# Optimization experiments

Measured on AMD Instinct MI355X. Metric: run time of the kernel, lower is better.

The kernel has to match this reference:

```python
import jax, jax.numpy as jnp
import numpy as np

M, K, N = 4096, 4096, 12288
GS = 128                 # quantization group size
G = K // GS              # number of groups
PACK = 8                 # int4 values per int32


def _pack_nibbles(key, shape_packed, axis_len):
    # generate random int4 values and pack 8 per int32 (bit-faithful GPTQ layout)
    nib = jax.random.randint(key, shape_packed[:1] + (PACK,) + shape_packed[1:], 0, 16, dtype=jnp.uint32)
    shifts = (jnp.arange(PACK, dtype=jnp.uint32) * 4)[None, :, None]
    return jnp.sum(nib << shifts, axis=1).astype(jnp.int32)


def setup_inputs() -> dict:
    key = jax.random.key(0)
    k1, k2, k3, k4, k5 = jax.random.split(key, 5)
    x = jax.random.normal(k1, (M, K), dtype=jnp.float32) * 0.05
    qweight = _pack_nibbles(k2, (K // PACK, N), K)          # [K/8, N] int32
    qzeros = _pack_nibbles(k3, (G, N // PACK), N)           # [G, N/8] int32
    scales = jax.random.uniform(k4, (G, N), dtype=jnp.float32, minval=0.001, maxval=0.01)
    bias = jax.random.normal(k5, (N,), dtype=jnp.float32) * 0.01
    return {"x": x, "qweight": qweight, "qzeros": qzeros, "scales": scales, "bias": bias}


def _unpack_rows(q):
    # [R, C] int32 -> [R*8, C] int4 values unpacked along rows
    shifts = (jnp.arange(PACK, dtype=jnp.uint32) * 4)[None, :, None]
    nib = (q.astype(jnp.uint32)[:, None, :] >> shifts) & jnp.uint32(0xF)
    return nib.reshape(q.shape[0] * PACK, q.shape[1])


def _unpack_cols(q):
    # [R, C] int32 -> [R, C*8] int4 values unpacked along columns
    shifts = (jnp.arange(PACK, dtype=jnp.uint32) * 4)[None, None, :]
    nib = (q.astype(jnp.uint32)[:, :, None] >> shifts) & jnp.uint32(0xF)
    return nib.reshape(q.shape[0], q.shape[1] * PACK)


def reference(x, qweight, qzeros, scales, bias):
    # dequantize: w[k,n] = (q[k,n] - (z[g,n]+1)) * s[g,n],  g = k // GS
    q = _unpack_rows(qweight).astype(jnp.float32)                    # [K, N]
    z = (_unpack_cols(qzeros).astype(jnp.float32) + 1.0)             # [G, N]
    s = scales                                                       # [G, N]
    w = (q.reshape(G, GS, N) - z[:, None, :]) * s[:, None, :]        # [G, GS, N]
    w = w.reshape(K, N)
    return x @ w + bias
```

## Files before the change

kernel.cpp:

```cpp
#include <hip/hip_runtime.h>
#include <hip/hip_bf16.h>

namespace {
constexpr int Md = 4096, Kd = 4096, Nd = 12288;
constexpr int BM = 256, BN = 128, BK = 64;
constexpr int TK = Kd / BK;
constexpr int THREADS = 512;
constexpr size_t A_BYTES = (size_t)Md * Kd * 2;
constexpr int AS_T = BM * BK;
constexpr int BS_T = BN * BK;
constexpr int LDS_BYTES = (2 * AS_T + BS_T) * 2;

typedef __attribute__((ext_vector_type(4))) float f4;
typedef __attribute__((ext_vector_type(8))) _Float16 h8;
typedef __attribute__((ext_vector_type(2))) _Float16 h2;

constexpr unsigned M4  = 0x000F000Fu;
constexpr unsigned MAG = 0x64006400u;

__device__ __forceinline__ unsigned pkrtz(float lo, float hi) {
  return __builtin_bit_cast(unsigned, __builtin_amdgcn_cvt_pkrtz(lo, hi));
}

__global__ __launch_bounds__(256)
void cvtA_kernel(const float* __restrict__ X, unsigned short* __restrict__ Xb, int n8) {
  int i = blockIdx.x * blockDim.x + threadIdx.x;
  const int stride = gridDim.x * blockDim.x;
  for (; i < n8; i += stride) {
    const f4* p = (const f4*)X + (size_t)i * 2;
    f4 a = p[0], b = p[1];
    uint4 o;
    o.x = pkrtz(a[0], b[0]);
    o.y = pkrtz(a[1], b[1]);
    o.z = pkrtz(a[2], b[2]);
    o.w = pkrtz(a[3], b[3]);
    ((uint4*)Xb)[i] = o;
  }
}

template<bool AWS>
__global__ __launch_bounds__(THREADS, 4)
void qgemm5(const float* __restrict__ X, const unsigned short* __restrict__ Xb,
            const int* __restrict__ QW, const int* __restrict__ QZ,
            const float* __restrict__ SC, const float* __restrict__ BS,
            float* __restrict__ OUT)
{
  extern __shared__ char smem[];
  unsigned short* As = (unsigned short*)smem;
  unsigned short* Bs = (unsigned short*)(smem + 2 * AS_T * 2);

  const int nwg = gridDim.x, cpx = nwg >> 3, b = blockIdx.x;
  const int swz = (b & 7) * cpx + (b >> 3);
  const int bm = swz / (Nd / BN), bn = swz % (Nd / BN);
  const int m0 = bm * BM, n0 = bn * BN;

  const int tid = threadIdx.x, lane = tid & 63, wid = tid >> 6;
  const int wr = wid >> 1, wc = wid & 1;
  const int n_l = tid & 127;
  const int k8b = (tid >> 7) * 2;
  const int nab = n0 + n_l;

  f4 acc[4][4];
  #pragma unroll
  for (int i = 0; i < 4; ++i)
    #pragma unroll
    for (int j = 0; j < 4; ++j) acc[i][j] = {0.0f, 0.0f, 0.0f, 0.0f};

  auto stageA = [&](int t, int buf) {
    #pragma unroll
    for (int i = 0; i < 4; ++i) {
      const int c = i * THREADS + tid;
      const int r = c >> 3, kbl = c & 7;
      const unsigned short* src = Xb + (size_t)(m0 + r) * Kd + t * BK + ((kbl ^ (r & 7)) << 3);
      __builtin_amdgcn_global_load_lds(
          (const __attribute__((address_space(1))) unsigned*)src,
          (__attribute__((address_space(3))) unsigned*)(As + buf * AS_T + c * 8),
          16, 0, 0);
    }
  };
  auto stageA_f = [&](int t, int buf) {
    #pragma unroll
    for (int i = 0; i < 4; ++i) {
      const int c = i * THREADS + tid;
      const int r = c >> 3, kbl = c & 7;
      const f4* src = (const f4*)(X + (size_t)(m0 + r) * Kd + t * BK + ((kbl ^ (r & 7)) << 3));
      f4 a = src[0], bb = src[1];
      uint4 o;
      o.x = pkrtz(a[0], bb[0]); o.y = pkrtz(a[1], bb[1]);
      o.z = pkrtz(a[2], bb[2]); o.w = pkrtz(a[3], bb[3]);
      *(uint4*)(As + buf * AS_T + c * 8) = o;
    }
  };

  auto loadB = [&](int t, int* w, unsigned& hs2, unsigned& hz2) {
    const int* qp = QW + (size_t)(t * 8 + k8b) * Nd + nab;
    w[0] = qp[0];
    w[1] = qp[Nd];
    const int g = t >> 1;
    const float s = SC[(size_t)g * Nd + nab];
    const int z32 = QZ[(size_t)g * (Nd / 8) + (nab >> 3)];
    const int z = (z32 >> ((nab & 7) * 4)) & 15;
    const unsigned hz = 0x6400u + (unsigned)z + 1u;
    hz2 = hz * 0x10001u;
    const unsigned short hs = __builtin_bit_cast(unsigned short, (_Float16)s);
    hs2 = (unsigned)hs * 0x10001u;
  };
  auto writeB = [&](const int* w, unsigned hs2, unsigned hz2) {
    const h2 vz = __builtin_bit_cast(h2, hz2);
    const h2 vs = __builtin_bit_cast(h2, hs2);
    #pragma unroll
    for (int i = 0; i < 2; ++i) {
      const unsigned q = (unsigned)w[i];
      const int k8 = k8b + i;
      const unsigned p0 = (q & M4) | MAG;
      const unsigned p1 = ((q >> 4) & M4) | MAG;
      const unsigned p2 = ((q >> 8) & M4) | MAG;
      const unsigned p3 = ((q >> 12) & M4) | MAG;
      const h2 f0 = (__builtin_bit_cast(h2, p0) - vz) * vs;
      const h2 f1 = (__builtin_bit_cast(h2, p1) - vz) * vs;
      const h2 f2 = (__builtin_bit_cast(h2, p2) - vz) * vs;
      const h2 f3 = (__builtin_bit_cast(h2, p3) - vz) * vs;
      uint4 o;
      o.x = __builtin_bit_cast(unsigned, f0);
      o.y = __builtin_bit_cast(unsigned, f1);
      o.z = __builtin_bit_cast(unsigned, f2);
      o.w = __builtin_bit_cast(unsigned, f3);
      *(uint4*)(Bs + n_l * BK + ((k8 ^ (n_l & 7)) << 3)) = o;
    }
  };

  auto mfma_tile = [&](int cb) {
    const unsigned short* Ab = As + cb * AS_T;
    #pragma unroll
    for (int ks = 0; ks < 2; ++ks) {
      h8 af[4], bf[4];
      const int kb = ks * 4 + (lane >> 4);
      #pragma unroll
      for (int mi = 0; mi < 4; ++mi) {
        const int r = wr * 64 + mi * 16 + (lane & 15);
        af[mi] = *(const h8*)&Ab[r * BK + ((kb ^ (r & 7)) << 3)];
      }
      #pragma unroll
      for (int ni = 0; ni < 4; ++ni) {
        const int cc = wc * 64 + ni * 16 + (lane & 15);
        bf[ni] = *(const h8*)&Bs[cc * BK + ((kb ^ (cc & 7)) << 3)];
      }
      #pragma unroll
      for (int mi = 0; mi < 4; ++mi)
        #pragma unroll
        for (int ni = 0; ni < 4; ++ni)
          acc[mi][ni] = __builtin_amdgcn_mfma_f32_16x16x32_f16(af[mi], bf[ni], acc[mi][ni], 0, 0, 0);
    }
  };

  int bw[2]; unsigned sHS, sHZ;
  int nbw[2]; unsigned nHS, nHZ;

  if constexpr (AWS) stageA(0, 0); else stageA_f(0, 0);
  loadB(0, bw, sHS, sHZ);
  writeB(bw, sHS, sHZ);
  __syncthreads();

  for (int t = 0; t < TK; ++t) {
    const int cb = t & 1;
    if (t + 1 < TK) {
      if constexpr (AWS) stageA(t + 1, cb ^ 1);
      loadB(t + 1, nbw, nHS, nHZ);
    }
    mfma_tile(cb);
    __syncthreads();
    if (t + 1 < TK) {
      if constexpr (!AWS) stageA_f(t + 1, cb ^ 1);
      writeB(nbw, nHS, nHZ);
    }
    __syncthreads();
  }

  #pragma unroll
  for (int ni = 0; ni < 4; ++ni) {
    const int gn = n0 + wc * 64 + ni * 16 + (lane & 15);
    const float bv = BS[gn];
    #pragma unroll
    for (int mi = 0; mi < 4; ++mi) {
      const int gm = m0 + wr * 64 + mi * 16 + ((lane >> 4) << 2);
      #pragma unroll
      for (int j = 0; j < 4; ++j)
        OUT[(size_t)(gm + j) * Nd + gn] = acc[mi][ni][j] + bv;
    }
  }
}
}

extern "C" void kernel_launch(void* const* d_in, const int* in_sizes, int n_in,
                              void* d_out, int out_size, void* d_ws, size_t ws_size,
                              hipStream_t stream) {
  const float* x  = (const float*)d_in[0];
  const int*   qw = (const int*)d_in[1];
  const int*   qz = (const int*)d_in[2];
  const float* sc = (const float*)d_in[3];
  const float* bs = (const float*)d_in[4];
  float* out = (float*)d_out;

  (void)hipFuncSetAttribute((const void*)qgemm5<true>,
                            hipFuncAttributeMaxDynamicSharedMemorySize, LDS_BYTES);
  (void)hipFuncSetAttribute((const void*)qgemm5<false>,
                            hipFuncAttributeMaxDynamicSharedMemorySize, LDS_BYTES);

  dim3 grid((Md / BM) * (Nd / BN));
  if (ws_size >= A_BYTES) {
    unsigned short* xb = (unsigned short*)d_ws;
    const int n8 = Md * Kd / 8;
    cvtA_kernel<<<2048, 256, 0, stream>>>(x, xb, n8);
    qgemm5<true><<<grid, dim3(THREADS), LDS_BYTES, stream>>>(x, xb, qw, qz, sc, bs, out);
  } else {
    qgemm5<false><<<grid, dim3(THREADS), LDS_BYTES, stream>>>(x, nullptr, qw, qz, sc, bs, out);
  }
}
```

Baseline: 419.3 us.

## Pre-dequantize weights to fp16 in workspace and run plain fp16 GEMM

Adds a separate kernel that dequantizes the int4 weights into an N-major fp16 buffer in the workspace. The main GEMM then streams both A and B into LDS with async global-to-LDS loads instead of dequantizing in registers each K step. The GEMM also moves to 256 threads, with each wave covering 128 rows and holding 8x4 accumulators. The aim is to take dequant ALU work and register staging out of the inner loop. The cost is an extra 96MB write and read of fp16 weights, more registers, and a larger workspace; when the workspace is too small the old path is kept as a fallback.

New measurement: 485.4 us. 1.16x slower.

```diff
diff --git a/kernel.cpp b/kernel.cpp
--- a/kernel.cpp
+++ b/kernel.cpp
@@ -5,11 +5,12 @@
 constexpr int Md = 4096, Kd = 4096, Nd = 12288;
 constexpr int BM = 256, BN = 128, BK = 64;
 constexpr int TK = Kd / BK;
-constexpr int THREADS = 512;
 constexpr size_t A_BYTES = (size_t)Md * Kd * 2;
+constexpr size_t W_BYTES = (size_t)Kd * Nd * 2;
 constexpr int AS_T = BM * BK;
 constexpr int BS_T = BN * BK;
-constexpr int LDS_BYTES = (2 * AS_T + BS_T) * 2;
+constexpr int LDS_MAIN = (2 * AS_T + BS_T) * 2;
+constexpr int LDS_FB   = (2 * AS_T + BS_T) * 2;
 
 typedef __attribute__((ext_vector_type(4))) float f4;
 typedef __attribute__((ext_vector_type(8))) _Float16 h8;
@@ -23,23 +24,168 @@
 }
 
 __global__ __launch_bounds__(256)
-void cvtA_kernel(const float* __restrict__ X, unsigned short* __restrict__ Xb, int n8) {
+void cvtA_nat(const float* __restrict__ X, unsigned short* __restrict__ Xb, int n8) {
   int i = blockIdx.x * blockDim.x + threadIdx.x;
   const int stride = gridDim.x * blockDim.x;
   for (; i < n8; i += stride) {
     const f4* p = (const f4*)X + (size_t)i * 2;
     f4 a = p[0], b = p[1];
     uint4 o;
-    o.x = pkrtz(a[0], b[0]);
-    o.y = pkrtz(a[1], b[1]);
-    o.z = pkrtz(a[2], b[2]);
-    o.w = pkrtz(a[3], b[3]);
+    o.x = pkrtz(a[0], a[1]); o.y = pkrtz(a[2], a[3]);
+    o.z = pkrtz(b[0], b[1]); o.w = pkrtz(b[2], b[3]);
     ((uint4*)Xb)[i] = o;
   }
 }
 
+__global__ __launch_bounds__(256)
+void cvtA_perm(const float* __restrict__ X, unsigned short* __restrict__ Xb, int n8) {
+  int i = blockIdx.x * blockDim.x + threadIdx.x;
+  const int stride = gridDim.x * blockDim.x;
+  for (; i < n8; i += stride) {
+    const f4* p = (const f4*)X + (size_t)i * 2;
+    f4 a = p[0], b = p[1];
+    uint4 o;
+    o.x = pkrtz(a[0], b[0]); o.y = pkrtz(a[1], b[1]);
+    o.z = pkrtz(a[2], b[2]); o.w = pkrtz(a[3], b[3]);
+    ((uint4*)Xb)[i] = o;
+  }
+}
+
+__global__ __launch_bounds__(256)
+void dequantW(const int* __restrict__ QW, const int* __restrict__ QZ,
+              const float* __restrict__ SC, unsigned short* __restrict__ Wt)
+{
+  __shared__ unsigned short L[64][68];
+  const int kb = blockIdx.x & 63;
+  const int nb = blockIdx.x >> 6;
+  const int g = kb >> 1;
+  const int t = threadIdx.x;
+  #pragma unroll
+  for (int i = 0; i < 2; ++i) {
+    const int idx = i * 256 + t;
+    const int k8l = idx >> 6, nl = idx & 63;
+    const int n = nb * 64 + nl;
+    const unsigned q = (unsigned)QW[(size_t)(kb * 8 + k8l) * Nd + n];
+    const float s = SC[(size_t)g * Nd + n];
+    const int z = (QZ[(size_t)g * (Nd / 8) + (n >> 3)] >> ((n & 7) * 4)) & 15;
+    const float negc = -(float)(z + 1) * s;
+    #pragma unroll
+    for (int j = 0; j < 8; ++j) {
+      const _Float16 v = (_Float16)__builtin_fmaf((float)((q >> (4 * j)) & 15u), s, negc);
+      L[nl][k8l * 8 + j] = __builtin_bit_cast(unsigned short, v);
+    }
+  }
+  __syncthreads();
+  #pragma unroll
+  for (int i = 0; i < 2; ++i) {
+    const int c = i * 256 + t;
+    const int nr = c >> 3, kc = c & 7;
+    const uint2 v0 = *(const uint2*)&L[nr][kc * 8];
+    const uint2 v1 = *(const uint2*)&L[nr][kc * 8 + 4];
+    uint4 v; v.x = v0.x; v.y = v0.y; v.z = v1.x; v.w = v1.y;
+    *(uint4*)&Wt[(size_t)(nb * 64 + nr) * Kd + kb * 64 + kc * 8] = v;
+  }
+}
+
+__global__ __launch_bounds__(256, 2)
+void qgemm6(const unsigned short* __restrict__ Xh, const unsigned short* __restrict__ Wt,
+            const float* __restrict__ BS, float* __restrict__ OUT)
+{
+  extern __shared__ char smem[];
+  unsigned short* As = (unsigned short*)smem;
+  unsigned short* Bs = (unsigned short*)(smem + 2 * AS_T * 2);
+
+  const int nwg = gridDim.x, cpx = nwg >> 3, b = blockIdx.x;
+  const int swz = (b & 7) * cpx + (b >> 3);
+  const int bm = swz & 15, bn = swz >> 4;
+  const int m0 = bm * BM, n0 = bn * BN;
+
+  const int tid = threadIdx.x, lane = tid & 63, wid = tid >> 6;
+  const int wr = wid >> 1, wc = wid & 1;
+
+  f4 acc[8][4];
+  #pragma unroll
+  for (int i = 0; i < 8; ++i)
+    #pragma unroll
+    for (int j = 0; j < 4; ++j) acc[i][j] = {0.0f, 0.0f, 0.0f, 0.0f};
+
+  auto stageA = [&](int t, int buf) {
+    #pragma unroll
+    for (int i = 0; i < 8; ++i) {
+      const int c = i * 256 + tid;
+      const int r = c >> 3, kbl = c & 7;
+      const unsigned short* src = Xh + (size_t)(m0 + r) * Kd + t * BK + ((kbl ^ (r & 7)) << 3);
+      __builtin_amdgcn_global_load_lds(
+          (const __attribute__((address_space(1))) unsigned*)src,
+          (__attribute__((address_space(3))) unsigned*)(As + buf * AS_T + c * 8),
+          16, 0, 0);
+    }
+  };
+  auto stageB = [&](int t) {
+    #pragma unroll
+    for (int i = 0; i < 4; ++i) {
+      const int c = i * 256 + tid;
+      const int r = c >> 3, kbl = c & 7;
+      const unsigned short* src = Wt + (size_t)(n0 + r) * Kd + t * BK + ((kbl ^ (r & 7)) << 3);
+      __builtin_amdgcn_global_load_lds(
+          (const __attribute__((address_space(1))) unsigned*)src,
+          (__attribute__((address_space(3))) unsigned*)(Bs + c * 8),
+          16, 0, 0);
+    }
+  };
+  auto mfma_tile = [&](int cb) {
+    const unsigned short* Ab = As + cb * AS_T;
+    #pragma unroll
+    for (int ks = 0; ks < 2; ++ks) {
+      h8 af[8], bf[4];
+      const int kb = ks * 4 + (lane >> 4);
+      #pragma unroll
+      for (int mi = 0; mi < 8; ++mi) {
+        const int r = wr * 128 + mi * 16 + (lane & 15);
+        af[mi] = *(const h8*)&Ab[r * BK + ((kb ^ (r & 7)) << 3)];
+      }
+      #pragma unroll
+      for (int ni = 0; ni < 4; ++ni) {
+        const int cc = wc * 64 + ni * 16 + (lane & 15);
+        bf[ni] = *(const h8*)&Bs[cc * BK + ((kb ^ (cc & 7)) << 3)];
+      }
+      #pragma unroll
+      for (int mi = 0; mi < 8; ++mi)
+        #pragma unroll
+        for (int ni = 0; ni < 4; ++ni)
+          acc[mi][ni] = __builtin_amdgcn_mfma_f32_16x16x32_f16(af[mi], bf[ni], acc[mi][ni], 0, 0, 0);
+    }
+  };
+
+  stageA(0, 0);
+  stageB(0);
+  __syncthreads();
+
+  for (int t = 0; t < TK; ++t) {
+    const int cb = t & 1;
+    if (t + 1 < TK) stageA(t + 1, cb ^ 1);
+    mfma_tile(cb);
+    __syncthreads();
+    if (t + 1 < TK) stageB(t + 1);
+    __syncthreads();
+  }
+
+  #pragma unroll
+  for (int ni = 0; ni < 4; ++ni) {
+    const int gn = n0 + wc * 64 + ni * 16 + (lane & 15);
+    const float bv = BS[gn];
+    #pragma unroll
+    for (int mi = 0; mi < 8; ++mi) {
+      const int gm = m0 + wr * 128 + mi * 16 + ((lane >> 4) << 2);
+      #pragma unroll
+      for (int j = 0; j < 4; ++j)
+        OUT[(size_t)(gm + j) * Nd + gn] = acc[mi][ni][j] + bv;
+    }
+  }
+}
+
 template<bool AWS>
-__global__ __launch_bounds__(THREADS, 4)
+__global__ __launch_bounds__(512, 4)
 void qgemm5(const float* __restrict__ X, const unsigned short* __restrict__ Xb,
             const int* __restrict__ QW, const int* __restrict__ QZ,
             const float* __restrict__ SC, const float* __restrict__ BS,
@@ -53,7 +199,6 @@
   const int swz = (b & 7) * cpx + (b >> 3);
   const int bm = swz / (Nd / BN), bn = swz % (Nd / BN);
   const int m0 = bm * BM, n0 = bn * BN;
-
   const int tid = threadIdx.x, lane = tid & 63, wid = tid >> 6;
   const int wr = wid >> 1, wc = wid & 1;
   const int n_l = tid & 127;
@@ -69,7 +214,7 @@
   auto stageA = [&](int t, int buf) {
     #pragma unroll
     for (int i = 0; i < 4; ++i) {
-      const int c = i * THREADS + tid;
+      const int c = i * 512 + tid;
       const int r = c >> 3, kbl = c & 7;
       const unsigned short* src = Xb + (size_t)(m0 + r) * Kd + t * BK + ((kbl ^ (r & 7)) << 3);
       __builtin_amdgcn_global_load_lds(
@@ -81,7 +226,7 @@
   auto stageA_f = [&](int t, int buf) {
     #pragma unroll
     for (int i = 0; i < 4; ++i) {
-      const int c = i * THREADS + tid;
+      const int c = i * 512 + tid;
       const int r = c >> 3, kbl = c & 7;
       const f4* src = (const f4*)(X + (size_t)(m0 + r) * Kd + t * BK + ((kbl ^ (r & 7)) << 3));
       f4 a = src[0], bb = src[1];
@@ -91,11 +236,9 @@
       *(uint4*)(As + buf * AS_T + c * 8) = o;
     }
   };
-
   auto loadB = [&](int t, int* w, unsigned& hs2, unsigned& hz2) {
     const int* qp = QW + (size_t)(t * 8 + k8b) * Nd + nab;
-    w[0] = qp[0];
-    w[1] = qp[Nd];
+    w[0] = qp[0]; w[1] = qp[Nd];
     const int g = t >> 1;
     const float s = SC[(size_t)g * Nd + nab];
     const int z32 = QZ[(size_t)g * (Nd / 8) + (nab >> 3)];
@@ -128,7 +271,6 @@
       *(uint4*)(Bs + n_l * BK + ((k8 ^ (n_l & 7)) << 3)) = o;
     }
   };
-
   auto mfma_tile = [&](int cb) {
     const unsigned short* Ab = As + cb * AS_T;
     #pragma unroll
@@ -175,7 +317,6 @@
     }
     __syncthreads();
   }
-
   #pragma unroll
   for (int ni = 0; ni < 4; ++ni) {
     const int gn = n0 + wc * 64 + ni * 16 + (lane & 15);
@@ -201,18 +342,26 @@
   const float* bs = (const float*)d_in[4];
   float* out = (float*)d_out;
 
+  (void)hipFuncSetAttribute((const void*)qgemm6,
+                            hipFuncAttributeMaxDynamicSharedMemorySize, LDS_MAIN);
   (void)hipFuncSetAttribute((const void*)qgemm5<true>,
-                            hipFuncAttributeMaxDynamicSharedMemorySize, LDS_BYTES);
+                            hipFuncAttributeMaxDynamicSharedMemorySize, LDS_FB);
   (void)hipFuncSetAttribute((const void*)qgemm5<false>,
-                            hipFuncAttributeMaxDynamicSharedMemorySize, LDS_BYTES);
+                            hipFuncAttributeMaxDynamicSharedMemorySize, LDS_FB);
 
   dim3 grid((Md / BM) * (Nd / BN));
-  if (ws_size >= A_BYTES) {
-    unsigned short* xb = (unsigned short*)d_ws;
-    const int n8 = Md * Kd / 8;
-    cvtA_kernel<<<2048, 256, 0, stream>>>(x, xb, n8);
-    qgemm5<true><<<grid, dim3(THREADS), LDS_BYTES, stream>>>(x, xb, qw, qz, sc, bs, out);
+  const int n8 = Md * Kd / 8;
+  if (ws_size >= A_BYTES + W_BYTES) {
+    unsigned short* xh = (unsigned short*)d_ws;
+    unsigned short* wt = (unsigned short*)((char*)d_ws + A_BYTES);
+    cvtA_nat<<<2048, 256, 0, stream>>>(x, xh, n8);
+    dequantW<<<(Kd / 64) * (Nd / 64), 256, 0, stream>>>(qw, qz, sc, wt);
+    qgemm6<<<grid, dim3(256), LDS_MAIN, stream>>>(xh, wt, bs, out);
+  } else if (ws_size >= A_BYTES) {
+    unsigned short* xh = (unsigned short*)d_ws;
+    cvtA_perm<<<2048, 256, 0, stream>>>(x, xh, n8);
+    qgemm5<true><<<grid, dim3(512), LDS_FB, stream>>>(x, xh, qw, qz, sc, bs, out);
   } else {
-    qgemm5<false><<<grid, dim3(THREADS), LDS_BYTES, stream>>>(x, nullptr, qw, qz, sc, bs, out);
-  }
-}
+    qgemm5<false><<<grid, dim3(512), LDS_FB, stream>>>(x, nullptr, qw, qz, sc, bs, out);
+  }
+}
```

## Drop A double buffering to cut LDS and raise occupancy target

Applied to the files above, without the earlier changes.

Removes the second LDS buffer for the A tile, shrinking shared memory per block. A staging now happens after the compute barrier instead of being prefetched during the MFMA loop. Launch bounds are raised to request more resident blocks. This trades load/compute overlap for higher occupancy and risks register pressure or spills from the tighter launch bound.

New measurement: 1.669 ms. 3.98x slower.

```diff
diff --git a/kernel.cpp b/kernel.cpp
--- a/kernel.cpp
+++ b/kernel.cpp
@@ -9,7 +9,7 @@
 constexpr size_t A_BYTES = (size_t)Md * Kd * 2;
 constexpr int AS_T = BM * BK;
 constexpr int BS_T = BN * BK;
-constexpr int LDS_BYTES = (2 * AS_T + BS_T) * 2;
+constexpr int LDS_BYTES = (AS_T + BS_T) * 2;
 
 typedef __attribute__((ext_vector_type(4))) float f4;
 typedef __attribute__((ext_vector_type(8))) _Float16 h8;
@@ -23,31 +23,29 @@
 }
 
 __global__ __launch_bounds__(256)
-void cvtA_kernel(const float* __restrict__ X, unsigned short* __restrict__ Xb, int n8) {
+void cvtA_perm(const float* __restrict__ X, unsigned short* __restrict__ Xb, int n8) {
   int i = blockIdx.x * blockDim.x + threadIdx.x;
   const int stride = gridDim.x * blockDim.x;
   for (; i < n8; i += stride) {
     const f4* p = (const f4*)X + (size_t)i * 2;
     f4 a = p[0], b = p[1];
     uint4 o;
-    o.x = pkrtz(a[0], b[0]);
-    o.y = pkrtz(a[1], b[1]);
-    o.z = pkrtz(a[2], b[2]);
-    o.w = pkrtz(a[3], b[3]);
+    o.x = pkrtz(a[0], b[0]); o.y = pkrtz(a[1], b[1]);
+    o.z = pkrtz(a[2], b[2]); o.w = pkrtz(a[3], b[3]);
     ((uint4*)Xb)[i] = o;
   }
 }
 
 template<bool AWS>
-__global__ __launch_bounds__(THREADS, 4)
-void qgemm5(const float* __restrict__ X, const unsigned short* __restrict__ Xb,
-            const int* __restrict__ QW, const int* __restrict__ QZ,
-            const float* __restrict__ SC, const float* __restrict__ BS,
-            float* __restrict__ OUT)
+__global__ __launch_bounds__(THREADS, 6)
+void qgemm13(const float* __restrict__ X, const unsigned short* __restrict__ Xb,
+             const int* __restrict__ QW, const int* __restrict__ QZ,
+             const float* __restrict__ SC, const float* __restrict__ BS,
+             float* __restrict__ OUT)
 {
   extern __shared__ char smem[];
   unsigned short* As = (unsigned short*)smem;
-  unsigned short* Bs = (unsigned short*)(smem + 2 * AS_T * 2);
+  unsigned short* Bs = (unsigned short*)(smem + AS_T * 2);
 
   const int nwg = gridDim.x, cpx = nwg >> 3, b = blockIdx.x;
   const int swz = (b & 7) * cpx + (b >> 3);
@@ -66,7 +64,7 @@
     #pragma unroll
     for (int j = 0; j < 4; ++j) acc[i][j] = {0.0f, 0.0f, 0.0f, 0.0f};
 
-  auto stageA = [&](int t, int buf) {
+  auto stageA = [&](int t) {
     #pragma unroll
     for (int i = 0; i < 4; ++i) {
       const int c = i * THREADS + tid;
@@ -74,11 +72,11 @@
       const unsigned short* src = Xb + (size_t)(m0 + r) * Kd + t * BK + ((kbl ^ (r & 7)) << 3);
       __builtin_amdgcn_global_load_lds(
           (const __attribute__((address_space(1))) unsigned*)src,
-          (__attribute__((address_space(3))) unsigned*)(As + buf * AS_T + c * 8),
+          (__attribute__((address_space(3))) unsigned*)(As + c * 8),
           16, 0, 0);
     }
   };
-  auto stageA_f = [&](int t, int buf) {
+  auto stageA_f = [&](int t) {
     #pragma unroll
     for (int i = 0; i < 4; ++i) {
       const int c = i * THREADS + tid;
@@ -88,7 +86,7 @@
       uint4 o;
       o.x = pkrtz(a[0], bb[0]); o.y = pkrtz(a[1], bb[1]);
       o.z = pkrtz(a[2], bb[2]); o.w = pkrtz(a[3], bb[3]);
-      *(uint4*)(As + buf * AS_T + c * 8) = o;
+      *(uint4*)(As + c * 8) = o;
     }
   };
 
@@ -100,10 +98,8 @@
     const float s = SC[(size_t)g * Nd + nab];
     const int z32 = QZ[(size_t)g * (Nd / 8) + (nab >> 3)];
     const int z = (z32 >> ((nab & 7) * 4)) & 15;
-    const unsigned hz = 0x6400u + (unsigned)z + 1u;
-    hz2 = hz * 0x10001u;
-    const unsigned short hs = __builtin_bit_cast(unsigned short, (_Float16)s);
-    hs2 = (unsigned)hs * 0x10001u;
+    hz2 = (0x6400u + (unsigned)z + 1u) * 0x10001u;
+    hs2 = (unsigned)__builtin_bit_cast(unsigned short, (_Float16)s) * 0x10001u;
   };
   auto writeB = [&](const int* w, unsigned hs2, unsigned hz2) {
     const h2 vz = __builtin_bit_cast(h2, hz2);
@@ -128,9 +124,7 @@
       *(uint4*)(Bs + n_l * BK + ((k8 ^ (n_l & 7)) << 3)) = o;
     }
   };
-
-  auto mfma_tile = [&](int cb) {
-    const unsigned short* Ab = As + cb * AS_T;
+  auto mfma_tile = [&]() {
     #pragma unroll
     for (int ks = 0; ks < 2; ++ks) {
       h8 af[4], bf[4];
@@ -138,7 +132,7 @@
       #pragma unroll
       for (int mi = 0; mi < 4; ++mi) {
         const int r = wr * 64 + mi * 16 + (lane & 15);
-        af[mi] = *(const h8*)&Ab[r * BK + ((kb ^ (r & 7)) << 3)];
+        af[mi] = *(const h8*)&As[r * BK + ((kb ^ (r & 7)) << 3)];
       }
       #pragma unroll
       for (int ni = 0; ni < 4; ++ni) {
@@ -156,21 +150,17 @@
   int bw[2]; unsigned sHS, sHZ;
   int nbw[2]; unsigned nHS, nHZ;
 
-  if constexpr (AWS) stageA(0, 0); else stageA_f(0, 0);
   loadB(0, bw, sHS, sHZ);
+  if constexpr (AWS) stageA(0); else stageA_f(0);
   writeB(bw, sHS, sHZ);
   __syncthreads();
 
   for (int t = 0; t < TK; ++t) {
-    const int cb = t & 1;
-    if (t + 1 < TK) {
-      if constexpr (AWS) stageA(t + 1, cb ^ 1);
-      loadB(t + 1, nbw, nHS, nHZ);
-    }
-    mfma_tile(cb);
+    if (t + 1 < TK) loadB(t + 1, nbw, nHS, nHZ);
+    mfma_tile();
     __syncthreads();
     if (t + 1 < TK) {
-      if constexpr (!AWS) stageA_f(t + 1, cb ^ 1);
+      if constexpr (AWS) stageA(t + 1); else stageA_f(t + 1);
       writeB(nbw, nHS, nHZ);
     }
     __syncthreads();
@@ -201,18 +191,18 @@
   const float* bs = (const float*)d_in[4];
   float* out = (float*)d_out;
 
-  (void)hipFuncSetAttribute((const void*)qgemm5<true>,
+  (void)hipFuncSetAttribute((const void*)qgemm13<true>,
                             hipFuncAttributeMaxDynamicSharedMemorySize, LDS_BYTES);
-  (void)hipFuncSetAttribute((const void*)qgemm5<false>,
+  (void)hipFuncSetAttribute((const void*)qgemm13<false>,
                             hipFuncAttributeMaxDynamicSharedMemorySize, LDS_BYTES);
 
   dim3 grid((Md / BM) * (Nd / BN));
   if (ws_size >= A_BYTES) {
-    unsigned short* xb = (unsigned short*)d_ws;
+    unsigned short* xh = (unsigned short*)d_ws;
     const int n8 = Md * Kd / 8;
-    cvtA_kernel<<<2048, 256, 0, stream>>>(x, xb, n8);
-    qgemm5<true><<<grid, dim3(THREADS), LDS_BYTES, stream>>>(x, xb, qw, qz, sc, bs, out);
+    cvtA_perm<<<2048, 256, 0, stream>>>(x, xh, n8);
+    qgemm13<true><<<grid, dim3(THREADS), LDS_BYTES, stream>>>(x, xh, qw, qz, sc, bs, out);
   } else {
-    qgemm5<false><<<grid, dim3(THREADS), LDS_BYTES, stream>>>(x, nullptr, qw, qz, sc, bs, out);
-  }
-}
+    qgemm13<false><<<grid, dim3(THREADS), LDS_BYTES, stream>>>(x, nullptr, qw, qz, sc, bs, out);
+  }
+}
```
